# Kernel optimization log

Hardware: AMD Instinct MI355X
Metric: run time of the kernel (lower is better)

## Reference

```python
import jax, jax.numpy as jnp
import numpy as np
import math

B, Q_LEN, K_LEN = 8, 512, 512
D_MODEL, H = 512, 8
DK = D_MODEL // H


def setup_inputs() -> dict:
    key = jax.random.key(0)
    ks = jax.random.split(key, 12)
    inp = {
        "query": jax.random.normal(ks[0], (B, Q_LEN, D_MODEL), jnp.float32),
        "key": jax.random.normal(ks[1], (B, K_LEN, D_MODEL), jnp.float32),
        "value": jax.random.normal(ks[2], (B, K_LEN, D_MODEL), jnp.float32),
        "relative_embeddings": jax.random.normal(ks[3], (K_LEN, Q_LEN, D_MODEL), jnp.float32),
        # causal mask: 1 = attend, 0 = masked
        "mask": jnp.tril(jnp.ones((Q_LEN, K_LEN), dtype=bool)),
        "Wq": jax.random.normal(ks[4], (D_MODEL, D_MODEL), jnp.float32) / math.sqrt(D_MODEL),
        "Wk": jax.random.normal(ks[5], (D_MODEL, D_MODEL), jnp.float32) / math.sqrt(D_MODEL),
        "Wv": jax.random.normal(ks[6], (D_MODEL, D_MODEL), jnp.float32) / math.sqrt(D_MODEL),
        "Wo": jax.random.normal(ks[7], (D_MODEL, D_MODEL), jnp.float32) / math.sqrt(D_MODEL),
        "Wr": jax.random.normal(ks[8], (D_MODEL, D_MODEL), jnp.float32) / math.sqrt(D_MODEL),
        "u": jax.random.normal(ks[9], (H, DK), jnp.float32),
        "v": jax.random.normal(ks[10], (H, DK), jnp.float32),
    }
    return inp


def reference(query, key, value, relative_embeddings, mask, Wq, Wk, Wv, Wo, Wr, u, v):
    b, q_len, d_model = query.shape
    k_len = key.shape[1]
    # torch nn.Linear(x) = x @ W.T (bias=False)
    Qh = (query @ Wq.T).reshape(b, q_len, H, DK).transpose(0, 2, 1, 3)   # bhqd
    Kh = (key @ Wk.T).reshape(b, k_len, H, DK).transpose(0, 2, 1, 3)     # bhkd
    Vh = (value @ Wv.T).reshape(b, k_len, H, DK).transpose(0, 2, 1, 3)   # bhkd
    # relative position projection: (k_len, q_len, d_model)
    R = relative_embeddings @ Wr.T
    # view(k,q,H,dk).permute(2,1,0,3) -> (H, q, k, dk)
    Rh = R.reshape(k_len, q_len, H, DK).transpose(2, 1, 0, 3)
    # content score: (Q + u) K^T
    content = jnp.einsum("bhqd,bhkd->bhqk", Qh + u[None, :, None, :], Kh)
    # position score: (Q + v) R^T, R per-head per-query
    position = jnp.einsum("bhqd,hqkd->bhqk", Qh + v[None, :, None, :], Rh)
    scores = (content + position) / math.sqrt(DK)
    scores = jnp.where(mask[None, None, :, :], scores, -1e9)
    weights = jax.nn.softmax(scores, axis=-1)  # dropout is identity in eval
    out = jnp.einsum("bhqk,bhkd->bhqd", weights, Vh)
    out = out.transpose(0, 2, 1, 3).reshape(b, q_len, d_model)
    out = out @ Wo.T
    return (out, weights)
```

## Files before the change

kernel.cpp:

```cpp
#include <hip/hip_runtime.h>

#define BATCH   8
#define SEQ     512
#define DMODEL  512
#define NHEAD   8
#define DKH     64

typedef __attribute__((ext_vector_type(8))) short bf16x8;
typedef __attribute__((ext_vector_type(4))) float f32x4;

__device__ __forceinline__ short f2bf(float f) {
    union { float f; unsigned u; } v; v.f = f;
    unsigned r = v.u + 0x7FFFu + ((v.u >> 16) & 1u);
    return (short)(r >> 16);
}
__device__ __forceinline__ float bf2f(short s) {
    union { unsigned u; float f; } v; v.u = ((unsigned)(unsigned short)s) << 16;
    return v.f;
}

#define LDK 40

__device__ __forceinline__ void stage_f32(const float* __restrict__ base,
                                          int rstride, short* lds, int tid) {
    int r = tid >> 2, c = (tid & 3) << 3;
    const float* p = base + (size_t)r * rstride + c;
    float4 x = *(const float4*)p;
    float4 y = *(const float4*)(p + 4);
    union { short s[8]; bf16x8 v; } o;
    o.s[0] = f2bf(x.x); o.s[1] = f2bf(x.y); o.s[2] = f2bf(x.z); o.s[3] = f2bf(x.w);
    o.s[4] = f2bf(y.x); o.s[5] = f2bf(y.y); o.s[6] = f2bf(y.z); o.s[7] = f2bf(y.w);
    *(bf16x8*)(lds + r * LDK + c) = o.v;
}

__device__ __forceinline__ void stage_bf16(const short* __restrict__ base,
                                           int rstride, short* lds, int tid) {
    int r = tid >> 2, c = (tid & 3) << 3;
    bf16x8 v = *(const bf16x8*)(base + (size_t)r * rstride + c);
    *(bf16x8*)(lds + r * LDK + c) = v;
}

__device__ __forceinline__ void mma_tile(const short* As, const short* Bs,
                                         int lane, int wm, int wn, f32x4 acc[2][2]) {
    int lo = lane & 15, hi = lane >> 4;
    bf16x8 a0 = *(const bf16x8*)(As + (wm * 32 + lo) * LDK + hi * 8);
    bf16x8 a1 = *(const bf16x8*)(As + (wm * 32 + 16 + lo) * LDK + hi * 8);
    bf16x8 b0 = *(const bf16x8*)(Bs + (wn * 32 + lo) * LDK + hi * 8);
    bf16x8 b1 = *(const bf16x8*)(Bs + (wn * 32 + 16 + lo) * LDK + hi * 8);
    acc[0][0] = __builtin_amdgcn_mfma_f32_16x16x32_bf16(a0, b0, acc[0][0], 0, 0, 0);
    acc[0][1] = __builtin_amdgcn_mfma_f32_16x16x32_bf16(a0, b1, acc[0][1], 0, 0, 0);
    acc[1][0] = __builtin_amdgcn_mfma_f32_16x16x32_bf16(a1, b0, acc[1][0], 0, 0, 0);
    acc[1][1] = __builtin_amdgcn_mfma_f32_16x16x32_bf16(a1, b1, acc[1][1], 0, 0, 0);
}

__global__ __launch_bounds__(256) void qkvw_kernel(
        const float* __restrict__ query, const float* __restrict__ key_,
        const float* __restrict__ value,
        const float* __restrict__ Wq, const float* __restrict__ Wk,
        const float* __restrict__ Wv, const float* __restrict__ Wr,
        const float* __restrict__ uvec, const float* __restrict__ vvec,
        short* __restrict__ Qu, short* __restrict__ Qv,
        short* __restrict__ Kh, short* __restrict__ Vt,
        short* __restrict__ Wrt) {
    __shared__ short As[64 * LDK], Bs[64 * LDK];
    int f = blockIdx.x, tid = threadIdx.x;
    if (f >= 1536) {
        int base = (f - 1536) * 1024;
        #pragma unroll
        for (int j = 0; j < 4; j++) {
            int idx = base + j * 256 + tid;
            int n = idx >> 9, m = idx & 511;
            Wrt[idx] = f2bf(Wr[(size_t)m * 512 + n]);
        }
        return;
    }
    int i = f >> 3;
    int nt = i & 7;
    int gm = (f & 7) * 24 + (i >> 3);
    int mode = gm >> 6, mt = gm & 63;
    const float* x = mode == 0 ? query : (mode == 1 ? key_ : value);
    const float* W = mode == 0 ? Wq : (mode == 1 ? Wk : Wv);
    int lane = tid & 63, w = tid >> 6, wm = w >> 1, wn = w & 1;
    const float* Abase = x + (size_t)mt * 64 * DMODEL;
    const float* Bbase = W + (size_t)nt * 64 * DMODEL;
    f32x4 acc[2][2] = {};
    for (int kt = 0; kt < DMODEL; kt += 32) {
        __syncthreads();
        stage_f32(Abase + kt, DMODEL, As, tid);
        stage_f32(Bbase + kt, DMODEL, Bs, tid);
        __syncthreads();
        mma_tile(As, Bs, lane, wm, wn, acc);
    }
    int lo = lane & 15, hi = lane >> 4;
    for (int fm = 0; fm < 2; fm++)
        for (int fn = 0; fn < 2; fn++)
            for (int r = 0; r < 4; r++) {
                int m = mt * 64 + wm * 32 + fm * 16 + hi * 4 + r;
                int n = nt * 64 + wn * 32 + fn * 16 + lo;
                float val = acc[fm][fn][r];
                int b = m >> 9, s = m & 511, h = n >> 6, d = n & 63;
                if (mode == 0) {
                    size_t idx = ((size_t)(b * NHEAD + h) * SEQ + s) * DKH + d;
                    Qu[idx] = f2bf(val + uvec[n]);
                    Qv[idx] = f2bf(val + vvec[n]);
                } else if (mode == 1) {
                    Kh[((size_t)(b * NHEAD + h) * SEQ + s) * DKH + d] = f2bf(val);
                } else {
                    Vt[((size_t)(b * NHEAD + h) * DKH + d) * SEQ + s] = f2bf(val);
                }
            }
}

__global__ __launch_bounds__(256) void tc_kernel(const short* __restrict__ Qv,
                                                 const short* __restrict__ Wrt,
                                                 short* __restrict__ T2,
                                                 const short* __restrict__ Qu,
                                                 const short* __restrict__ Kh,
                                                 float* __restrict__ scores) {
    __shared__ short As[64 * LDK], Bs[64 * LDK];
    int f0 = blockIdx.x, tid = threadIdx.x;
    int lane = tid & 63, w = tid >> 6, wm = w >> 1, wn = w & 1;
    int lo = lane & 15, hi = lane >> 4;
    if (f0 < 4096) {
        int f = f0;
        int i = f >> 3;
        int nt = i & 7;
        int mh = (f & 7) * 64 + (i >> 3);
        int mt = mh >> 3, h = mh & 7;
        int m0 = mt * 64, b = m0 >> 9, q0 = m0 & 511;
        const short* Abase = Qv + ((size_t)(b * NHEAD + h) * SEQ + q0) * DKH;
        const short* Bbase = Wrt + (size_t)nt * 64 * DMODEL + h * DKH;
        f32x4 acc[2][2] = {};
        for (int kt = 0; kt < DKH; kt += 32) {
            __syncthreads();
            stage_bf16(Abase + kt, DKH, As, tid);
            stage_bf16(Bbase + kt, DMODEL, Bs, tid);
            __syncthreads();
            mma_tile(As, Bs, lane, wm, wn, acc);
        }
        int bh = b * NHEAD + h;
        for (int fm = 0; fm < 2; fm++)
            for (int fn = 0; fn < 2; fn++)
                for (int r = 0; r < 4; r++) {
                    int q = q0 + wm * 32 + fm * 16 + hi * 4 + r;
                    int n = nt * 64 + wn * 32 + fn * 16 + lo;
                    T2[((size_t)q * 64 + bh) * DMODEL + n] = f2bf(acc[fm][fn][r]);
                }
    } else {
        int f = f0 - 4096;
        int i = f >> 3;
        int bh = (f & 7) * 8 + (i >> 6);
        int rest = i & 63;
        int kt_ = rest & 7, qt = rest >> 3;
        if (kt_ > qt) return;
        const short* Abase = Qu + ((size_t)bh * SEQ + qt * 64) * DKH;
        const short* Bbase = Kh + ((size_t)bh * SEQ + kt_ * 64) * DKH;
        f32x4 acc[2][2] = {};
        for (int kt = 0; kt < DKH; kt += 32) {
            __syncthreads();
            stage_bf16(Abase + kt, DKH, As, tid);
            stage_bf16(Bbase + kt, DKH, Bs, tid);
            __syncthreads();
            mma_tile(As, Bs, lane, wm, wn, acc);
        }
        for (int fm = 0; fm < 2; fm++)
            for (int fn = 0; fn < 2; fn++)
                for (int r = 0; r < 4; r++) {
                    int q = qt * 64 + wm * 32 + fm * 16 + hi * 4 + r;
                    int k = kt_ * 64 + wn * 32 + fn * 16 + lo;
                    scores[((size_t)bh * SEQ + q) * SEQ + k] = acc[fm][fn][r];
                }
    }
}

__global__ __launch_bounds__(1024) void position_kernel(const short* __restrict__ T2,
                                                        const float* __restrict__ rel,
                                                        float* __restrict__ scores) {
    int bk = blockIdx.x;
    int x = bk & 7, idx = bk >> 3;
    int q = (idx < 32) ? (idx * 8 + x) : (511 - ((idx - 32) * 8 + x));
    __shared__ short Tl[64 * 512];
    int tid = threadIdx.x, w = tid >> 6, lane = tid & 63;
    const short* Tq = T2 + (size_t)q * (64 * DMODEL);
    #pragma unroll
    for (int it = 0; it < 4; ++it) {
        int chunk = it * 1024 + tid;
        int r = chunk >> 6, c = chunk & 63;
        bf16x8 v = *(const bf16x8*)(Tq + (size_t)chunk * 8);
        *(bf16x8*)(Tl + r * 512 + (c ^ (r & 7)) * 8) = v;
    }
    __syncthreads();
    int kbase = w * 32;
    if (kbase > q) return;
    int lo = lane & 15, hi = lane >> 4;
    const float* relq = rel + ((size_t)kbase * SEQ + q) * DMODEL;
    f32x4 acc[4][2] = {};
    for (int n = 0; n < DMODEL; n += 32) {
        bf16x8 a[4];
        #pragma unroll
        for (int fm = 0; fm < 4; fm++) {
            int rr = fm * 16 + lo;
            int g = ((n >> 3) + hi) ^ (rr & 7);
            a[fm] = *(const bf16x8*)(Tl + rr * 512 + g * 8);
        }
        bf16x8 bfrag[2];
        #pragma unroll
        for (int fk = 0; fk < 2; fk++) {
            const float* p = relq + (size_t)(fk * 16 + lo) * (SEQ * DMODEL) + n + hi * 8;
            float4 xv = *(const float4*)p;
            float4 yv = *(const float4*)(p + 4);
            union { short s[8]; bf16x8 v; } o;
            o.s[0] = f2bf(xv.x); o.s[1] = f2bf(xv.y); o.s[2] = f2bf(xv.z); o.s[3] = f2bf(xv.w);
            o.s[4] = f2bf(yv.x); o.s[5] = f2bf(yv.y); o.s[6] = f2bf(yv.z); o.s[7] = f2bf(yv.w);
            bfrag[fk] = o.v;
        }
        #pragma unroll
        for (int fm = 0; fm < 4; fm++) {
            acc[fm][0] = __builtin_amdgcn_mfma_f32_16x16x32_bf16(a[fm], bfrag[0], acc[fm][0], 0, 0, 0);
            acc[fm][1] = __builtin_amdgcn_mfma_f32_16x16x32_bf16(a[fm], bfrag[1], acc[fm][1], 0, 0, 0);
        }
    }
    #pragma unroll
    for (int fm = 0; fm < 4; fm++)
        #pragma unroll
        for (int fk = 0; fk < 2; fk++)
            #pragma unroll
            for (int r = 0; r < 4; r++) {
                int bh = fm * 16 + hi * 4 + r;
                int k = kbase + fk * 16 + lo;
                scores[((size_t)bh * SEQ + q) * SEQ + k] += acc[fm][fk][r];
            }
}

#define PSTR 520
__global__ __launch_bounds__(256) void pv_sm_kernel(float* __restrict__ scores,
                                                    const short* __restrict__ Vt,
                                                    short* __restrict__ attn) {
    __shared__ short Ps[64 * PSTR];
    __shared__ float invS_lds[64];
    int f = blockIdx.x;
    int i = f >> 3;
    int bh = (f & 7) * 8 + (i >> 3);
    int qt = i & 7;
    int tid = threadIdx.x, lane = tid & 63, w = tid >> 6, wm = w >> 1, wn = w & 1;
    int kmax = (qt + 1) * 64;
    int r = tid >> 2, c4 = tid & 3;
    int q = qt * 64 + r;
    int cc = c4 * 8;
    float* row = scores + ((size_t)bh * SEQ + q) * SEQ;
    float S = 0.f;
    for (int kt = 0; kt < kmax; kt += 32) {
        float4 x = *(const float4*)(row + kt + cc);
        float4 y = *(const float4*)(row + kt + cc + 4);
        float p0 = (kt + cc + 0 <= q) ? __expf(x.x * 0.125f) : 0.f;
        float p1 = (kt + cc + 1 <= q) ? __expf(x.y * 0.125f) : 0.f;
        float p2 = (kt + cc + 2 <= q) ? __expf(x.z * 0.125f) : 0.f;
        float p3 = (kt + cc + 3 <= q) ? __expf(x.w * 0.125f) : 0.f;
        float p4 = (kt + cc + 4 <= q) ? __expf(y.x * 0.125f) : 0.f;
        float p5 = (kt + cc + 5 <= q) ? __expf(y.y * 0.125f) : 0.f;
        float p6 = (kt + cc + 6 <= q) ? __expf(y.z * 0.125f) : 0.f;
        float p7 = (kt + cc + 7 <= q) ? __expf(y.w * 0.125f) : 0.f;
        S += p0 + p1 + p2 + p3 + p4 + p5 + p6 + p7;
        union { short s[8]; bf16x8 v; } o;
        o.s[0] = f2bf(p0); o.s[1] = f2bf(p1); o.s[2] = f2bf(p2); o.s[3] = f2bf(p3);
        o.s[4] = f2bf(p4); o.s[5] = f2bf(p5); o.s[6] = f2bf(p6); o.s[7] = f2bf(p7);
        *(bf16x8*)(Ps + r * PSTR + kt + cc) = o.v;
    }
    S += __shfl_xor(S, 1); S += __shfl_xor(S, 2);
    float invS = 1.0f / S;
    if (c4 == 0) invS_lds[r] = invS;
    for (int kt = 0; kt < SEQ; kt += 32) {
        float4 o0, o1;
        if (kt < kmax) {
            const short* pr = Ps + r * PSTR + kt + cc;
            o0 = make_float4(bf2f(pr[0]) * invS, bf2f(pr[1]) * invS,
                             bf2f(pr[2]) * invS, bf2f(pr[3]) * invS);
            o1 = make_float4(bf2f(pr[4]) * invS, bf2f(pr[5]) * invS,
                             bf2f(pr[6]) * invS, bf2f(pr[7]) * invS);
        } else {
            o0 = make_float4(0.f, 0.f, 0.f, 0.f); o1 = o0;
        }
        *(float4*)(row + kt + cc) = o0;
        *(float4*)(row + kt + cc + 4) = o1;
    }
    __syncthreads();
    const short* Vtb = Vt + (size_t)bh * DKH * SEQ;
    int lo = lane & 15, hi = lane >> 4;
    f32x4 acc[2][2] = {};
    for (int kc = 0; kc < kmax; kc += 32) {
        bf16x8 a0 = *(const bf16x8*)(Ps + (wm * 32 + lo) * PSTR + kc + hi * 8);
        bf16x8 a1 = *(const bf16x8*)(Ps + (wm * 32 + 16 + lo) * PSTR + kc + hi * 8);
        bf16x8 b0 = *(const bf16x8*)(Vtb + (size_t)(wn * 32 + lo) * SEQ + kc + hi * 8);
        bf16x8 b1 = *(const bf16x8*)(Vtb + (size_t)(wn * 32 + 16 + lo) * SEQ + kc + hi * 8);
        acc[0][0] = __builtin_amdgcn_mfma_f32_16x16x32_bf16(a0, b0, acc[0][0], 0, 0, 0);
        acc[0][1] = __builtin_amdgcn_mfma_f32_16x16x32_bf16(a0, b1, acc[0][1], 0, 0, 0);
        acc[1][0] = __builtin_amdgcn_mfma_f32_16x16x32_bf16(a1, b0, acc[1][0], 0, 0, 0);
        acc[1][1] = __builtin_amdgcn_mfma_f32_16x16x32_bf16(a1, b1, acc[1][1], 0, 0, 0);
    }
    int b = bh >> 3, h = bh & 7;
    for (int fm = 0; fm < 2; fm++)
        for (int fn = 0; fn < 2; fn++)
            for (int rr = 0; rr < 4; rr++) {
                int ql = wm * 32 + fm * 16 + hi * 4 + rr;
                int d = wn * 32 + fn * 16 + lo;
                float val = acc[fm][fn][rr] * invS_lds[ql];
                attn[((size_t)b * SEQ + qt * 64 + ql) * DMODEL + h * DKH + d] = f2bf(val);
            }
}

__global__ __launch_bounds__(256) void oproj_kernel(const short* __restrict__ attn,
                                                    const float* __restrict__ Wo,
                                                    float* __restrict__ out) {
    __shared__ short As[64 * LDK], Bs[64 * LDK];
    int f = blockIdx.x;
    int i = f >> 3;
    int mt = (f & 7) * 8 + (i >> 3);
    int nt = i & 7;
    int tid = threadIdx.x, lane = tid & 63, w = tid >> 6, wm = w >> 1, wn = w & 1;
    const short* Abase = attn + (size_t)mt * 64 * DMODEL;
    const float* Bbase = Wo + (size_t)nt * 64 * DMODEL;
    f32x4 acc[2][2] = {};
    for (int kt = 0; kt < DMODEL; kt += 32) {
        __syncthreads();
        stage_bf16(Abase + kt, DMODEL, As, tid);
        stage_f32(Bbase + kt, DMODEL, Bs, tid);
        __syncthreads();
        mma_tile(As, Bs, lane, wm, wn, acc);
    }
    int lo = lane & 15, hi = lane >> 4;
    for (int fm = 0; fm < 2; fm++)
        for (int fn = 0; fn < 2; fn++)
            for (int r = 0; r < 4; r++) {
                int m = mt * 64 + wm * 32 + fm * 16 + hi * 4 + r;
                int n = nt * 64 + wn * 32 + fn * 16 + lo;
                out[(size_t)m * DMODEL + n] = acc[fm][fn][r];
            }
}

extern "C" void kernel_launch(void* const* d_in, const int* in_sizes, int n_in,
                              void* d_out, int out_size, void* d_ws, size_t ws_size,
                              hipStream_t stream) {
    (void)in_sizes; (void)n_in; (void)out_size; (void)ws_size;
    const float* query = (const float*)d_in[0];
    const float* key   = (const float*)d_in[1];
    const float* value = (const float*)d_in[2];
    const float* rel   = (const float*)d_in[3];
    const float* Wq = (const float*)d_in[5];
    const float* Wk = (const float*)d_in[6];
    const float* Wv = (const float*)d_in[7];
    const float* Wo = (const float*)d_in[8];
    const float* Wr = (const float*)d_in[9];
    const float* u  = (const float*)d_in[10];
    const float* v  = (const float*)d_in[11];

    float* out     = (float*)d_out;
    float* weights = out + (size_t)BATCH * SEQ * DMODEL;

    char* ws = (char*)d_ws;
    short* Qu   = (short*)(ws);
    short* Qv   = (short*)(ws + ((size_t)4 << 20));
    short* Kh   = (short*)(ws + ((size_t)8 << 20));
    short* Vt   = (short*)(ws + ((size_t)12 << 20));
    short* T2   = (short*)(ws + ((size_t)16 << 20));
    short* attn = (short*)(ws + ((size_t)48 << 20));
    short* Wrt  = (short*)(ws + ((size_t)52 << 20));

    qkvw_kernel<<<1792, 256, 0, stream>>>(query, key, value, Wq, Wk, Wv, Wr,
                                          u, v, Qu, Qv, Kh, Vt, Wrt);
    tc_kernel<<<8192, 256, 0, stream>>>(Qv, Wrt, T2, Qu, Kh, weights);
    position_kernel<<<512, 1024, 0, stream>>>(T2, rel, weights);
    pv_sm_kernel<<<512, 256, 0, stream>>>(weights, Vt, attn);
    oproj_kernel<<<512, 256, 0, stream>>>(attn, Wo, out);
}
```

Baseline: 194.6 us.

## Fuse Qv·Wr projection into position kernel, drop T2 global intermediate

Moves the computation of T2 (Qv projected through the head slice of Wr) out of the combined tc_kernel and into position_kernel, where each block computes its query's 64x512 T tile directly into LDS with MFMA. The global write and read of the 32 MB T2 buffer are removed, and tc_kernel becomes a content-only kernel. In exchange, every position block re-reads Wr (512x512 bf16) from global/L2 and does extra MFMA work before its main loop, which may lengthen the position kernel's critical path.

```diff
diff --git a/kernel.cpp b/kernel.cpp
--- a/kernel.cpp
+++ b/kernel.cpp
@@ -111,88 +111,85 @@
             }
 }
 
-__global__ __launch_bounds__(256) void tc_kernel(const short* __restrict__ Qv,
-                                                 const short* __restrict__ Wrt,
-                                                 short* __restrict__ T2,
-                                                 const short* __restrict__ Qu,
-                                                 const short* __restrict__ Kh,
-                                                 float* __restrict__ scores) {
+__global__ __launch_bounds__(256) void content_kernel(const short* __restrict__ Qu,
+                                                      const short* __restrict__ Kh,
+                                                      float* __restrict__ scores) {
+    int f = blockIdx.x;
+    int i = f >> 3;
+    int bh = (f & 7) * 8 + (i >> 6);
+    int rest = i & 63;
+    int kt_ = rest & 7, qt = rest >> 3;
+    if (kt_ > qt) return;
     __shared__ short As[64 * LDK], Bs[64 * LDK];
-    int f0 = blockIdx.x, tid = threadIdx.x;
-    int lane = tid & 63, w = tid >> 6, wm = w >> 1, wn = w & 1;
-    int lo = lane & 15, hi = lane >> 4;
-    if (f0 < 4096) {
-        int f = f0;
-        int i = f >> 3;
-        int nt = i & 7;
-        int mh = (f & 7) * 64 + (i >> 3);
-        int mt = mh >> 3, h = mh & 7;
-        int m0 = mt * 64, b = m0 >> 9, q0 = m0 & 511;
-        const short* Abase = Qv + ((size_t)(b * NHEAD + h) * SEQ + q0) * DKH;
-        const short* Bbase = Wrt + (size_t)nt * 64 * DMODEL + h * DKH;
-        f32x4 acc[2][2] = {};
-        for (int kt = 0; kt < DKH; kt += 32) {
-            __syncthreads();
-            stage_bf16(Abase + kt, DKH, As, tid);
-            stage_bf16(Bbase + kt, DMODEL, Bs, tid);
-            __syncthreads();
-            mma_tile(As, Bs, lane, wm, wn, acc);
-        }
-        int bh = b * NHEAD + h;
-        for (int fm = 0; fm < 2; fm++)
-            for (int fn = 0; fn < 2; fn++)
-                for (int r = 0; r < 4; r++) {
-                    int q = q0 + wm * 32 + fm * 16 + hi * 4 + r;
-                    int n = nt * 64 + wn * 32 + fn * 16 + lo;
-                    T2[((size_t)q * 64 + bh) * DMODEL + n] = f2bf(acc[fm][fn][r]);
-                }
-    } else {
-        int f = f0 - 4096;
-        int i = f >> 3;
-        int bh = (f & 7) * 8 + (i >> 6);
-        int rest = i & 63;
-        int kt_ = rest & 7, qt = rest >> 3;
-        if (kt_ > qt) return;
-        const short* Abase = Qu + ((size_t)bh * SEQ + qt * 64) * DKH;
-        const short* Bbase = Kh + ((size_t)bh * SEQ + kt_ * 64) * DKH;
-        f32x4 acc[2][2] = {};
-        for (int kt = 0; kt < DKH; kt += 32) {
-            __syncthreads();
-            stage_bf16(Abase + kt, DKH, As, tid);
-            stage_bf16(Bbase + kt, DKH, Bs, tid);
-            __syncthreads();
-            mma_tile(As, Bs, lane, wm, wn, acc);
-        }
-        for (int fm = 0; fm < 2; fm++)
-            for (int fn = 0; fn < 2; fn++)
-                for (int r = 0; r < 4; r++) {
-                    int q = qt * 64 + wm * 32 + fm * 16 + hi * 4 + r;
-                    int k = kt_ * 64 + wn * 32 + fn * 16 + lo;
-                    scores[((size_t)bh * SEQ + q) * SEQ + k] = acc[fm][fn][r];
-                }
-    }
-}
-
-__global__ __launch_bounds__(1024) void position_kernel(const short* __restrict__ T2,
+    int tid = threadIdx.x, lane = tid & 63, w = tid >> 6, wm = w >> 1, wn = w & 1;
+    const short* Abase = Qu + ((size_t)bh * SEQ + qt * 64) * DKH;
+    const short* Bbase = Kh + ((size_t)bh * SEQ + kt_ * 64) * DKH;
+    f32x4 acc[2][2] = {};
+    for (int kt = 0; kt < DKH; kt += 32) {
+        __syncthreads();
+        stage_bf16(Abase + kt, DKH, As, tid);
+        stage_bf16(Bbase + kt, DKH, Bs, tid);
+        __syncthreads();
+        mma_tile(As, Bs, lane, wm, wn, acc);
+    }
+    int lo = lane & 15, hi = lane >> 4;
+    for (int fm = 0; fm < 2; fm++)
+        for (int fn = 0; fn < 2; fn++)
+            for (int r = 0; r < 4; r++) {
+                int q = qt * 64 + wm * 32 + fm * 16 + hi * 4 + r;
+                int k = kt_ * 64 + wn * 32 + fn * 16 + lo;
+                scores[((size_t)bh * SEQ + q) * SEQ + k] = acc[fm][fn][r];
+            }
+}
+
+__global__ __launch_bounds__(1024) void position_kernel(const short* __restrict__ Qv,
+                                                        const short* __restrict__ Wrt,
                                                         const float* __restrict__ rel,
                                                         float* __restrict__ scores) {
     int bk = blockIdx.x;
     int x = bk & 7, idx = bk >> 3;
     int q = (idx < 32) ? (idx * 8 + x) : (511 - ((idx - 32) * 8 + x));
     __shared__ short Tl[64 * 512];
+    __shared__ short Qs[64 * 72];
     int tid = threadIdx.x, w = tid >> 6, lane = tid & 63;
-    const short* Tq = T2 + (size_t)q * (64 * DMODEL);
-    #pragma unroll
-    for (int it = 0; it < 4; ++it) {
-        int chunk = it * 1024 + tid;
-        int r = chunk >> 6, c = chunk & 63;
-        bf16x8 v = *(const bf16x8*)(Tq + (size_t)chunk * 8);
-        *(bf16x8*)(Tl + r * 512 + (c ^ (r & 7)) * 8) = v;
+    int lo = lane & 15, hi = lane >> 4;
+    if (tid < 512) {
+        int bh = tid >> 3, j = tid & 7;
+        bf16x8 v = *(const bf16x8*)(Qv + ((size_t)bh * SEQ + q) * DKH + j * 8);
+        *(bf16x8*)(Qs + bh * 72 + j * 8) = v;
+    }
+    __syncthreads();
+    {
+        int h = w >> 1, halfm = w & 1;
+        int nb = halfm * 256;
+        int bh = (lo & 7) * 8 + h;
+        bf16x8 bfrag[2];
+        #pragma unroll
+        for (int ks = 0; ks < 2; ks++)
+            bfrag[ks] = *(const bf16x8*)(Qs + bh * 72 + ks * 32 + hi * 8);
+        #pragma unroll
+        for (int fm = 0; fm < 16; fm++) {
+            f32x4 tacc = {};
+            #pragma unroll
+            for (int ks = 0; ks < 2; ks++) {
+                bf16x8 afrag = *(const bf16x8*)(Wrt + (size_t)(nb + fm * 16 + lo) * DMODEL
+                                                + h * 64 + ks * 32 + hi * 8);
+                tacc = __builtin_amdgcn_mfma_f32_16x16x32_bf16(afrag, bfrag[ks], tacc, 0, 0, 0);
+            }
+            if (lo < 8) {
+                int n0 = nb + fm * 16 + hi * 4;
+                unsigned long long u =
+                      (unsigned long long)(unsigned short)f2bf(tacc[0])
+                    | ((unsigned long long)(unsigned short)f2bf(tacc[1]) << 16)
+                    | ((unsigned long long)(unsigned short)f2bf(tacc[2]) << 32)
+                    | ((unsigned long long)(unsigned short)f2bf(tacc[3]) << 48);
+                *(unsigned long long*)(Tl + bh * 512 + ((n0 >> 3) ^ (bh & 7)) * 8 + (n0 & 7)) = u;
+            }
+        }
     }
     __syncthreads();
     int kbase = w * 32;
     if (kbase > q) return;
-    int lo = lane & 15, hi = lane >> 4;
     const float* relq = rel + ((size_t)kbase * SEQ + q) * DMODEL;
     f32x4 acc[4][2] = {};
     for (int n = 0; n < DMODEL; n += 32) {
@@ -361,14 +358,13 @@
     short* Qv   = (short*)(ws + ((size_t)4 << 20));
     short* Kh   = (short*)(ws + ((size_t)8 << 20));
     short* Vt   = (short*)(ws + ((size_t)12 << 20));
-    short* T2   = (short*)(ws + ((size_t)16 << 20));
-    short* attn = (short*)(ws + ((size_t)48 << 20));
-    short* Wrt  = (short*)(ws + ((size_t)52 << 20));
+    short* attn = (short*)(ws + ((size_t)16 << 20));
+    short* Wrt  = (short*)(ws + ((size_t)20 << 20));
 
     qkvw_kernel<<<1792, 256, 0, stream>>>(query, key, value, Wq, Wk, Wv, Wr,
                                           u, v, Qu, Qv, Kh, Vt, Wrt);
-    tc_kernel<<<8192, 256, 0, stream>>>(Qv, Wrt, T2, Qu, Kh, weights);
-    position_kernel<<<512, 1024, 0, stream>>>(T2, rel, weights);
+    content_kernel<<<4096, 256, 0, stream>>>(Qu, Kh, weights);
+    position_kernel<<<512, 1024, 0, stream>>>(Qv, Wrt, rel, weights);
     pv_sm_kernel<<<512, 256, 0, stream>>>(weights, Vt, attn);
     oproj_kernel<<<512, 256, 0, stream>>>(attn, Wo, out);
 }
```

Result: slower. 206.9 us, median of 2 (+6.3%).
